# Kernel optimization log

Measured on AMD Instinct MI355X. Metric: run time of the kernel, lower is better.

## Reference

```python
import jax, jax.numpy as jnp
import numpy as np

B, N, F, L = 4, 8192, 64, 2


def setup_inputs() -> dict:
    key = jax.random.key(0)
    k1, k2, k3 = jax.random.split(key, 3)
    x = jax.random.normal(k1, (B, N, F), dtype=jnp.float32)
    net_params = jax.random.normal(k2, (L * F * F,), dtype=jnp.float32)
    A = jax.random.normal(k3, (N, N), dtype=jnp.float32)
    return {"x": x, "t": 0, "net_params": net_params, "A": A}


def reference(x, t, net_params, A):
    # weights: [L, F, F]
    weights = net_params.reshape(L, F, F)
    # x: [B, N, F] (original does x.view(-1, A.size(1), features))
    z = x.reshape(-1, A.shape[1], F)
    for i in range(L):
        # GCN_operation: Z_out = A @ Z @ W_i  (the nested vmm loops emulate exactly this)
        h = jnp.einsum('mn,bnf->bmf', A, z)          # [B, N, F]
        z = jnp.einsum('bmf,fg->bmg', h, weights[i])  # [B, N, F]
        z = jax.nn.relu(z)
    return z
```

## Files before the change

kernel.cpp:

```cpp
#include <hip/hip_runtime.h>
#include <stdint.h>


#define MK 8192

typedef float f32x4 __attribute__((ext_vector_type(4)));
typedef uint32_t u32x4 __attribute__((ext_vector_type(4)));
typedef uint32_t u32x2 __attribute__((ext_vector_type(2)));
typedef __bf16 bf16x8 __attribute__((ext_vector_type(8)));

__device__ inline uint16_t f2bf(float f) {
  uint32_t u = __builtin_bit_cast(uint32_t, f);
  u += 0x7fffu + ((u >> 16) & 1u);
  return (uint16_t)(u >> 16);
}

#define GLD(src, dstbase)                                                                    \
  __builtin_amdgcn_global_load_lds((const __attribute__((address_space(1))) uint32_t*)(src), \
                                   (__attribute__((address_space(3))) uint32_t*)(dstbase),   \
                                   16, 0, 0)

__global__ __launch_bounds__(256) void zw0(const float* __restrict__ x,
                                           const float* __restrict__ net,
                                           uint16_t* __restrict__ Zt) {
  __shared__ float Wl[64 * 64];
  __shared__ float rows[64][65];
  const int b = blockIdx.y, n0 = blockIdx.x * 64, tid = threadIdx.x;
  for (int i = tid * 4; i < 4096; i += 1024) {
    f32x4 v = *(const f32x4*)(net + i);
    Wl[i] = v[0]; Wl[i + 1] = v[1]; Wl[i + 2] = v[2]; Wl[i + 3] = v[3];
  }
  const float* src = x + ((uint64_t)b * MK + n0) * 64;
  for (int i = tid * 4; i < 4096; i += 1024) {
    f32x4 v = *(const f32x4*)(src + i);
    int r = i >> 6, f = i & 63;
    rows[r][f] = v[0]; rows[r][f + 1] = v[1]; rows[r][f + 2] = v[2]; rows[r][f + 3] = v[3];
  }
  __syncthreads();
  const int nl = tid & 63, g0 = (tid >> 6) * 16;
  float s[16];
#pragma unroll
  for (int j = 0; j < 16; ++j) s[j] = 0.f;
  for (int f = 0; f < 64; ++f) {
    float rv = rows[nl][f];
#pragma unroll
    for (int j = 0; j < 16; ++j) s[j] = fmaf(rv, Wl[f * 64 + g0 + j], s[j]);
  }
  uint16_t* dst = Zt + (uint64_t)(b * 64 + g0) * MK + n0 + nl;
#pragma unroll
  for (int j = 0; j < 16; ++j) dst[(uint64_t)j * MK] = f2bf(s[j]);
}

__global__ __launch_bounds__(512, 2) void gemm1(const float* __restrict__ Af,
                                                const uint16_t* __restrict__ Bt,
                                                uint16_t* __restrict__ Ab,
                                                float* __restrict__ P) {
  __shared__ __align__(16) uint16_t As[2][16384];
  __shared__ __align__(16) uint16_t Bs[2][16384];
  const int bid = (int)blockIdx.x;
  const int s = bid & 7, bm = bid >> 3;
  const int row0 = bm * 256, k0 = s * 1024;
  const int tid = threadIdx.x, wid = tid >> 6, lane = tid & 63;
  const int wr = wid >> 2, wc = wid & 3;

  const int lsub = lane >> 3;
  const int ksrc = ((lane & 7) ^ lsub) << 3;
  const uint16_t* gB0 = Bt + (uint64_t)(4 * wid * 8 + lsub) * MK + k0 + ksrc;
  const int lBo = 4 * wid * 512;

  const int arow = (8 * wid) * 4 + (lane >> 4);
  const int acol = (lane & 15) * 4;
  const float* gA0 = Af + (uint64_t)(row0 + arow) * MK + k0 + acol;
  const int koct = (lane & 15) >> 1, krem = (lane & 1) * 4;

  f32x4 acc[8][4] = {};
  f32x4 rv[8];

  auto loadA = [&](int kofs) {
#pragma unroll
    for (int j = 0; j < 8; ++j)
      rv[j] = __builtin_nontemporal_load((const f32x4*)(gA0 + (uint64_t)j * 4 * MK + kofs));
  };
  auto stageA = [&](int buf, int kofs) {
#pragma unroll
    for (int j = 0; j < 8; ++j) {
      const int r = arow + j * 4;
      u32x2 w;
      w[0] = (uint32_t)f2bf(rv[j][0]) | ((uint32_t)f2bf(rv[j][1]) << 16);
      w[1] = (uint32_t)f2bf(rv[j][2]) | ((uint32_t)f2bf(rv[j][3]) << 16);
      *(u32x2*)&As[buf][r * 64 + ((koct ^ (r & 7)) << 3) + krem] = w;
      *(u32x2*)(Ab + (uint64_t)(row0 + r) * MK + k0 + kofs + acol) = w;
    }
  };

  loadA(0);
#pragma unroll
  for (int j = 0; j < 4; ++j) GLD(gB0 + (uint64_t)j * 8 * MK, &Bs[0][lBo + j * 512]);
  stageA(0, 0);
  __syncthreads();

  int buf = 0;
  for (int t = 0; t < 16; ++t) {
    const int nxt = (t + 1) * 64;
    if (t < 15) {
      loadA(nxt);
#pragma unroll
      for (int j = 0; j < 4; ++j) GLD(gB0 + (uint64_t)j * 8 * MK + nxt, &Bs[buf ^ 1][lBo + j * 512]);
    }
#pragma unroll
    for (int kk = 0; kk < 2; ++kk) {
      const int kb = kk * 4 + (lane >> 4);
      bf16x8 a[8], b[4];
#pragma unroll
      for (int mi = 0; mi < 8; ++mi) {
        const int r = wr * 128 + mi * 16 + (lane & 15);
        a[mi] = *(const bf16x8*)&As[buf][r * 64 + ((kb ^ (r & 7)) << 3)];
      }
#pragma unroll
      for (int n = 0; n < 4; ++n) {
        const int r = wc * 64 + n * 16 + (lane & 15);
        b[n] = *(const bf16x8*)&Bs[buf][r * 64 + ((kb ^ (r & 7)) << 3)];
      }
#pragma unroll
      for (int mi = 0; mi < 8; ++mi)
#pragma unroll
        for (int n = 0; n < 4; ++n)
          acc[mi][n] = __builtin_amdgcn_mfma_f32_16x16x32_bf16(a[mi], b[n], acc[mi][n], 0, 0, 0);
    }
    if (t < 15) stageA(buf ^ 1, nxt);
    __syncthreads();
    buf ^= 1;
  }

  float* Pp = P + (uint64_t)s * 2097152;
  const int lr = (lane >> 4) * 4, lc = lane & 15;
#pragma unroll
  for (int mi = 0; mi < 8; ++mi)
#pragma unroll
    for (int n = 0; n < 4; ++n) {
      const int gr = row0 + wr * 128 + mi * 16 + lr;
      const int gc = wc * 64 + n * 16 + lc;
#pragma unroll
      for (int j = 0; j < 4; ++j)
        Pp[(uint64_t)(gr + j) * 256 + gc] = acc[mi][n][j];
    }
}

__global__ __launch_bounds__(512, 2) void gemm2(const uint16_t* __restrict__ Ab,
                                                const uint16_t* __restrict__ Bt,
                                                float* __restrict__ P) {
  __shared__ __align__(16) uint16_t As[2][16384];
  __shared__ __align__(16) uint16_t Bs[2][16384];
  const int bid = (int)blockIdx.x;
  const int s = bid & 7, bm = bid >> 3;
  const int row0 = bm * 256, k0 = s * 1024;
  const int tid = threadIdx.x, wid = tid >> 6, lane = tid & 63;
  const int wr = wid >> 2, wc = wid & 3;

  const int lsub = lane >> 3;
  const int ksrc = ((lane & 7) ^ lsub) << 3;
  const uint16_t* gA0 = Ab + (uint64_t)(row0 + 4 * wid * 8 + lsub) * MK + k0 + ksrc;
  const uint16_t* gB0 = Bt + (uint64_t)(4 * wid * 8 + lsub) * MK + k0 + ksrc;
  const int lo = 4 * wid * 512;

  f32x4 acc[8][4] = {};

#pragma unroll
  for (int j = 0; j < 4; ++j) {
    GLD(gA0 + (uint64_t)j * 8 * MK, &As[0][lo + j * 512]);
    GLD(gB0 + (uint64_t)j * 8 * MK, &Bs[0][lo + j * 512]);
  }
  __syncthreads();

  int buf = 0;
  for (int t = 0; t < 16; ++t) {
    if (t < 15) {
      const int nxt = (t + 1) * 64;
#pragma unroll
      for (int j = 0; j < 4; ++j) {
        GLD(gA0 + (uint64_t)j * 8 * MK + nxt, &As[buf ^ 1][lo + j * 512]);
        GLD(gB0 + (uint64_t)j * 8 * MK + nxt, &Bs[buf ^ 1][lo + j * 512]);
      }
    }
#pragma unroll
    for (int kk = 0; kk < 2; ++kk) {
      const int kb = kk * 4 + (lane >> 4);
      bf16x8 a[8], b[4];
#pragma unroll
      for (int mi = 0; mi < 8; ++mi) {
        const int r = wr * 128 + mi * 16 + (lane & 15);
        a[mi] = *(const bf16x8*)&As[buf][r * 64 + ((kb ^ (r & 7)) << 3)];
      }
#pragma unroll
      for (int n = 0; n < 4; ++n) {
        const int r = wc * 64 + n * 16 + (lane & 15);
        b[n] = *(const bf16x8*)&Bs[buf][r * 64 + ((kb ^ (r & 7)) << 3)];
      }
#pragma unroll
      for (int mi = 0; mi < 8; ++mi)
#pragma unroll
        for (int n = 0; n < 4; ++n)
          acc[mi][n] = __builtin_amdgcn_mfma_f32_16x16x32_bf16(a[mi], b[n], acc[mi][n], 0, 0, 0);
    }
    __syncthreads();
    buf ^= 1;
  }

  float* Pp = P + (uint64_t)s * 2097152;
  const int lr = (lane >> 4) * 4, lc = lane & 15;
#pragma unroll
  for (int mi = 0; mi < 8; ++mi)
#pragma unroll
    for (int n = 0; n < 4; ++n) {
      const int gr = row0 + wr * 128 + mi * 16 + lr;
      const int gc = wc * 64 + n * 16 + lc;
#pragma unroll
      for (int j = 0; j < 4; ++j)
        Pp[(uint64_t)(gr + j) * 256 + gc] = acc[mi][n][j];
    }
}

__global__ __launch_bounds__(256) void zw1P(const float* __restrict__ P,
                                            const float* __restrict__ net,
                                            uint16_t* __restrict__ Zt) {
  __shared__ float Wl[64 * 64];
  __shared__ float rows[64][65];
  const int b = blockIdx.y, n0 = blockIdx.x * 64, tid = threadIdx.x;
  const float* Wsrc = net + 4096;
  for (int i = tid * 4; i < 4096; i += 1024) {
    f32x4 v = *(const f32x4*)(Wsrc + i);
    Wl[i] = v[0]; Wl[i + 1] = v[1]; Wl[i + 2] = v[2]; Wl[i + 3] = v[3];
  }
#pragma unroll
  for (int g = 0; g < 4; ++g) {
    const int idx = (tid + g * 256) * 4;
    const int r = idx >> 6, f0 = idx & 63;
    const float* base = P + (uint64_t)(n0 + r) * 256 + b * 64 + f0;
    f32x4 v = *(const f32x4*)base;
#pragma unroll
    for (int s = 1; s < 8; ++s) v += *(const f32x4*)(base + (uint64_t)s * 2097152);
#pragma unroll
    for (int j = 0; j < 4; ++j) rows[r][f0 + j] = fmaxf(v[j], 0.0f);
  }
  __syncthreads();
  const int nl = tid & 63, g0 = (tid >> 6) * 16;
  float s[16];
#pragma unroll
  for (int j = 0; j < 16; ++j) s[j] = 0.f;
  for (int f = 0; f < 64; ++f) {
    float rv = rows[nl][f];
#pragma unroll
    for (int j = 0; j < 16; ++j) s[j] = fmaf(rv, Wl[f * 64 + g0 + j], s[j]);
  }
  uint16_t* dst = Zt + (uint64_t)(b * 64 + g0) * MK + n0 + nl;
#pragma unroll
  for (int j = 0; j < 16; ++j) dst[(uint64_t)j * MK] = f2bf(s[j]);
}

__global__ __launch_bounds__(256) void combineF(const float* __restrict__ P,
                                                float* __restrict__ out) {
  const uint64_t e = ((uint64_t)blockIdx.x * 256 + threadIdx.x) * 4;
  f32x4 v = *(const f32x4*)&P[e];
#pragma unroll
  for (int s = 1; s < 8; ++s) v += *(const f32x4*)&P[(uint64_t)s * 2097152 + e];
#pragma unroll
  for (int j = 0; j < 4; ++j) v[j] = fmaxf(v[j], 0.0f);
  const int m = (int)(e >> 8);
  const int c = (int)(e & 255);
  *(f32x4*)&out[(((uint64_t)(c >> 6)) * MK + m) * 64 + (c & 63)] = v;
}

extern "C" void kernel_launch(void* const* d_in, const int* in_sizes, int n_in,
                              void* d_out, int out_size, void* d_ws, size_t ws_size,
                              hipStream_t stream) {
  const float* x   = (const float*)d_in[0];
  const float* net = (const float*)d_in[2];
  const float* A   = (const float*)d_in[3];
  float* out = (float*)d_out;

  uint16_t* Ab = (uint16_t*)d_ws;
  uint16_t* Zt = (uint16_t*)((char*)d_ws + 134217728ull);
  float*    P  = (float*)   ((char*)d_ws + 142606336ull);

  zw0<<<dim3(128, 4), dim3(256), 0, stream>>>(x, net, Zt);
  gemm1<<<dim3(256), dim3(512), 0, stream>>>(A, Zt, Ab, P);
  zw1P<<<dim3(128, 4), dim3(256), 0, stream>>>(P, net, Zt);
  gemm2<<<dim3(256), dim3(512), 0, stream>>>(Ab, Zt, P);
  combineF<<<dim3(2048), dim3(256), 0, stream>>>(P, out);
}
```

Before: 184.1 us.

## Store split-K partials in bf16 and restructure gemm2 pipeline scheduling

Measured after the change: 172.0 us. 1.07x faster.

```diff
diff --git a/kernel.cpp b/kernel.cpp
--- a/kernel.cpp
+++ b/kernel.cpp
@@ -13,6 +13,9 @@
   uint32_t u = __builtin_bit_cast(uint32_t, f);
   u += 0x7fffu + ((u >> 16) & 1u);
   return (uint16_t)(u >> 16);
+}
+__device__ inline float bf2f(uint32_t lo16) {
+  return __builtin_bit_cast(float, lo16 << 16);
 }
 
 #define GLD(src, dstbase)                                                                    \
@@ -54,7 +57,7 @@
 __global__ __launch_bounds__(512, 2) void gemm1(const float* __restrict__ Af,
                                                 const uint16_t* __restrict__ Bt,
                                                 uint16_t* __restrict__ Ab,
-                                                float* __restrict__ P) {
+                                                uint16_t* __restrict__ P) {
   __shared__ __align__(16) uint16_t As[2][16384];
   __shared__ __align__(16) uint16_t Bs[2][16384];
   const int bid = (int)blockIdx.x;
@@ -132,7 +135,7 @@
     buf ^= 1;
   }
 
-  float* Pp = P + (uint64_t)s * 2097152;
+  uint16_t* Pp = P + (uint64_t)s * 2097152;
   const int lr = (lane >> 4) * 4, lc = lane & 15;
 #pragma unroll
   for (int mi = 0; mi < 8; ++mi)
@@ -142,13 +145,13 @@
       const int gc = wc * 64 + n * 16 + lc;
 #pragma unroll
       for (int j = 0; j < 4; ++j)
-        Pp[(uint64_t)(gr + j) * 256 + gc] = acc[mi][n][j];
+        Pp[(uint64_t)(gr + j) * 256 + gc] = f2bf(acc[mi][n][j]);
     }
 }
 
 __global__ __launch_bounds__(512, 2) void gemm2(const uint16_t* __restrict__ Ab,
                                                 const uint16_t* __restrict__ Bt,
-                                                float* __restrict__ P) {
+                                                uint16_t* __restrict__ P) {
   __shared__ __align__(16) uint16_t As[2][16384];
   __shared__ __align__(16) uint16_t Bs[2][16384];
   const int bid = (int)blockIdx.x;
@@ -170,43 +173,56 @@
     GLD(gA0 + (uint64_t)j * 8 * MK, &As[0][lo + j * 512]);
     GLD(gB0 + (uint64_t)j * 8 * MK, &Bs[0][lo + j * 512]);
   }
-  __syncthreads();
 
   int buf = 0;
   for (int t = 0; t < 16; ++t) {
-    if (t < 15) {
-      const int nxt = (t + 1) * 64;
-#pragma unroll
-      for (int j = 0; j < 4; ++j) {
-        GLD(gA0 + (uint64_t)j * 8 * MK + nxt, &As[buf ^ 1][lo + j * 512]);
-        GLD(gB0 + (uint64_t)j * 8 * MK + nxt, &Bs[buf ^ 1][lo + j * 512]);
+    const int tko = ((t + 1) < 16 ? (t + 1) : 15) * 64;
+#pragma unroll
+    for (int j = 0; j < 4; ++j) {
+      GLD(gA0 + (uint64_t)j * 8 * MK + tko, &As[buf ^ 1][lo + j * 512]);
+      GLD(gB0 + (uint64_t)j * 8 * MK + tko, &Bs[buf ^ 1][lo + j * 512]);
+    }
+    asm volatile("s_waitcnt vmcnt(8)" ::: "memory");
+    __builtin_amdgcn_s_barrier();
+    __builtin_amdgcn_sched_barrier(0);
+
+    bf16x8 b[4][2];
+#pragma unroll
+    for (int n = 0; n < 4; ++n)
+#pragma unroll
+      for (int kk = 0; kk < 2; ++kk) {
+        const int r = wc * 64 + n * 16 + (lane & 15);
+        const int kb = kk * 4 + (lane >> 4);
+        b[n][kk] = *(const bf16x8*)&Bs[buf][r * 64 + ((kb ^ (r & 7)) << 3)];
       }
-    }
-#pragma unroll
-    for (int kk = 0; kk < 2; ++kk) {
-      const int kb = kk * 4 + (lane >> 4);
-      bf16x8 a[8], b[4];
-#pragma unroll
-      for (int mi = 0; mi < 8; ++mi) {
-        const int r = wr * 128 + mi * 16 + (lane & 15);
-        a[mi] = *(const bf16x8*)&As[buf][r * 64 + ((kb ^ (r & 7)) << 3)];
-      }
-#pragma unroll
-      for (int n = 0; n < 4; ++n) {
-        const int r = wc * 64 + n * 16 + (lane & 15);
-        b[n] = *(const bf16x8*)&Bs[buf][r * 64 + ((kb ^ (r & 7)) << 3)];
-      }
-#pragma unroll
-      for (int mi = 0; mi < 8; ++mi)
-#pragma unroll
-        for (int n = 0; n < 4; ++n)
-          acc[mi][n] = __builtin_amdgcn_mfma_f32_16x16x32_bf16(a[mi], b[n], acc[mi][n], 0, 0, 0);
-    }
-    __syncthreads();
+#pragma unroll
+    for (int q = 0; q < 4; ++q) {
+      bf16x8 a[2][2];
+#pragma unroll
+      for (int i = 0; i < 2; ++i)
+#pragma unroll
+        for (int kk = 0; kk < 2; ++kk) {
+          const int r = wr * 128 + (2 * q + i) * 16 + (lane & 15);
+          const int kb = kk * 4 + (lane >> 4);
+          a[i][kk] = *(const bf16x8*)&As[buf][r * 64 + ((kb ^ (r & 7)) << 3)];
+        }
+      __builtin_amdgcn_s_setprio(1);
+#pragma unroll
+      for (int kk = 0; kk < 2; ++kk)
+#pragma unroll
+        for (int i = 0; i < 2; ++i)
+#pragma unroll
+          for (int n = 0; n < 4; ++n)
+            acc[2 * q + i][n] =
+                __builtin_amdgcn_mfma_f32_16x16x32_bf16(a[i][kk], b[n][kk], acc[2 * q + i][n], 0, 0, 0);
+      __builtin_amdgcn_s_setprio(0);
+      __builtin_amdgcn_sched_barrier(0);
+    }
+    __builtin_amdgcn_s_barrier();
     buf ^= 1;
   }
 
-  float* Pp = P + (uint64_t)s * 2097152;
+  uint16_t* Pp = P + (uint64_t)s * 2097152;
   const int lr = (lane >> 4) * 4, lc = lane & 15;
 #pragma unroll
   for (int mi = 0; mi < 8; ++mi)
@@ -216,11 +232,11 @@
       const int gc = wc * 64 + n * 16 + lc;
 #pragma unroll
       for (int j = 0; j < 4; ++j)
-        Pp[(uint64_t)(gr + j) * 256 + gc] = acc[mi][n][j];
-    }
-}
-
-__global__ __launch_bounds__(256) void zw1P(const float* __restrict__ P,
+        Pp[(uint64_t)(gr + j) * 256 + gc] = f2bf(acc[mi][n][j]);
+    }
+}
+
+__global__ __launch_bounds__(256) void zw1P(const uint16_t* __restrict__ P,
                                             const float* __restrict__ net,
                                             uint16_t* __restrict__ Zt) {
   __shared__ float Wl[64 * 64];
@@ -232,15 +248,22 @@
     Wl[i] = v[0]; Wl[i + 1] = v[1]; Wl[i + 2] = v[2]; Wl[i + 3] = v[3];
   }
 #pragma unroll
-  for (int g = 0; g < 4; ++g) {
-    const int idx = (tid + g * 256) * 4;
+  for (int g = 0; g < 2; ++g) {
+    const int idx = (tid + g * 256) * 8;
     const int r = idx >> 6, f0 = idx & 63;
-    const float* base = P + (uint64_t)(n0 + r) * 256 + b * 64 + f0;
-    f32x4 v = *(const f32x4*)base;
-#pragma unroll
-    for (int s = 1; s < 8; ++s) v += *(const f32x4*)(base + (uint64_t)s * 2097152);
-#pragma unroll
-    for (int j = 0; j < 4; ++j) rows[r][f0 + j] = fmaxf(v[j], 0.0f);
+    const uint16_t* base = P + (uint64_t)(n0 + r) * 256 + b * 64 + f0;
+    float acc8[8] = {};
+#pragma unroll
+    for (int sp = 0; sp < 8; ++sp) {
+      u32x4 v = *(const u32x4*)(base + (uint64_t)sp * 2097152);
+#pragma unroll
+      for (int j = 0; j < 4; ++j) {
+        acc8[2 * j]     += bf2f(v[j] & 0xffffu);
+        acc8[2 * j + 1] += bf2f(v[j] >> 16);
+      }
+    }
+#pragma unroll
+    for (int j = 0; j < 8; ++j) rows[r][f0 + j] = fmaxf(acc8[j], 0.0f);
   }
   __syncthreads();
   const int nl = tid & 63, g0 = (tid >> 6) * 16;
@@ -257,17 +280,27 @@
   for (int j = 0; j < 16; ++j) dst[(uint64_t)j * MK] = f2bf(s[j]);
 }
 
-__global__ __launch_bounds__(256) void combineF(const float* __restrict__ P,
+__global__ __launch_bounds__(256) void combineF(const uint16_t* __restrict__ P,
                                                 float* __restrict__ out) {
-  const uint64_t e = ((uint64_t)blockIdx.x * 256 + threadIdx.x) * 4;
-  f32x4 v = *(const f32x4*)&P[e];
-#pragma unroll
-  for (int s = 1; s < 8; ++s) v += *(const f32x4*)&P[(uint64_t)s * 2097152 + e];
-#pragma unroll
-  for (int j = 0; j < 4; ++j) v[j] = fmaxf(v[j], 0.0f);
+  const uint64_t e = ((uint64_t)blockIdx.x * 256 + threadIdx.x) * 8;
+  float acc8[8] = {};
+#pragma unroll
+  for (int sp = 0; sp < 8; ++sp) {
+    u32x4 v = *(const u32x4*)&P[(uint64_t)sp * 2097152 + e];
+#pragma unroll
+    for (int j = 0; j < 4; ++j) {
+      acc8[2 * j]     += bf2f(v[j] & 0xffffu);
+      acc8[2 * j + 1] += bf2f(v[j] >> 16);
+    }
+  }
   const int m = (int)(e >> 8);
   const int c = (int)(e & 255);
-  *(f32x4*)&out[(((uint64_t)(c >> 6)) * MK + m) * 64 + (c & 63)] = v;
+  float* dst = &out[(((uint64_t)(c >> 6)) * MK + m) * 64 + (c & 63)];
+  f32x4 w0, w1;
+#pragma unroll
+  for (int j = 0; j < 4; ++j) { w0[j] = fmaxf(acc8[j], 0.0f); w1[j] = fmaxf(acc8[4 + j], 0.0f); }
+  *(f32x4*)dst = w0;
+  *(f32x4*)(dst + 4) = w1;
 }
 
 extern "C" void kernel_launch(void* const* d_in, const int* in_sizes, int n_in,
@@ -280,11 +313,11 @@
 
   uint16_t* Ab = (uint16_t*)d_ws;
   uint16_t* Zt = (uint16_t*)((char*)d_ws + 134217728ull);
-  float*    P  = (float*)   ((char*)d_ws + 142606336ull);
+  uint16_t* P  = (uint16_t*)((char*)d_ws + 142606336ull);
 
   zw0<<<dim3(128, 4), dim3(256), 0, stream>>>(x, net, Zt);
   gemm1<<<dim3(256), dim3(512), 0, stream>>>(A, Zt, Ab, P);
   zw1P<<<dim3(128, 4), dim3(256), 0, stream>>>(P, net, Zt);
   gemm2<<<dim3(256), dim3(512), 0, stream>>>(Ab, Zt, P);
-  combineF<<<dim3(2048), dim3(256), 0, stream>>>(P, out);
-}
+  combineF<<<dim3(1024), dim3(256), 0, stream>>>(P, out);
+}
```
